# Optimization experiments

Measured on AMD Instinct MI355X. Metric: run time of the kernel, lower is better.

Reference implementation:

```python
import jax, jax.numpy as jnp
import numpy as np
import math

B, S, H, NH = 2, 2048, 2048, 16
HD = H // NH
BASE = 10000.0


def _rope_tables():
    inv_freq = 1.0 / (BASE ** (np.arange(0, HD, 2, dtype=np.float32) / HD))
    t = np.arange(S, dtype=np.float32)
    freqs = np.einsum('i,j->ij', t, inv_freq)          # [S, HD/2]
    emb = np.concatenate([freqs, freqs], axis=-1)       # [S, HD]
    return jnp.asarray(np.cos(emb)), jnp.asarray(np.sin(emb))


def setup_inputs() -> dict:
    key = jax.random.key(0)
    ks = jax.random.split(key, 6)
    scale = 1.0 / math.sqrt(H)
    cos, sin = _rope_tables()
    causal = np.triu(np.full((S, S), -1e9, dtype=np.float32), k=1)
    attn_bias = jnp.broadcast_to(jnp.asarray(causal)[None, None], (B, 1, S, S))
    return {
        'hidden_states': jax.random.normal(ks[0], (B, S, H), jnp.float32),
        'masks': jnp.zeros((B, S, S), jnp.float32),
        'attn_bias': attn_bias,
        'cos': cos,
        'sin': sin,
        'wq': jax.random.normal(ks[1], (H, H), jnp.float32) * scale,
        'wk': jax.random.normal(ks[2], (H, H), jnp.float32) * scale,
        'wv': jax.random.normal(ks[3], (H, H), jnp.float32) * scale,
        'wo': jax.random.normal(ks[4], (H, H), jnp.float32) * scale,
        'position_ids': jnp.broadcast_to(jnp.arange(S, dtype=jnp.int64)[None], (B, S)),
    }


def _rotate_half(x):
    x1, x2 = x[..., : x.shape[-1] // 2], x[..., x.shape[-1] // 2:]
    return jnp.concatenate([-x2, x1], axis=-1)


def reference(hidden_states, masks, attn_bias, cos, sin, wq, wk, wv, wo, position_ids):
    b, s, h = hidden_states.shape
    nh, hd = NH, HD
    # QKV projections (torch Linear: x @ W.T), split heads -> [b, nh, s, hd]
    def proj(w):
        return (hidden_states @ w.T).reshape(b, s, nh, hd).transpose(0, 2, 1, 3)
    q, k, v = proj(wq), proj(wk), proj(wv)
    # RoPE
    cos_p = cos[position_ids][:, None]  # [b, 1, s, hd]
    sin_p = sin[position_ids][:, None]
    q = q * cos_p + _rotate_half(q) * sin_p
    k = k * cos_p + _rotate_half(k) * sin_p
    # attention scores with additive masks (mx_attn branch, fp math)
    att = jnp.einsum('bhqd,bhkd->bhqk', q / math.sqrt(hd), k)
    att = att + attn_bias + masks[:, None]
    att = jax.nn.softmax(att, axis=-1)
    out = jnp.einsum('bhqk,bhkd->bhqd', att, v)
    out = out.transpose(0, 2, 1, 3).reshape(b, s, h)
    return out @ wo.T
```

## Files before the change

kernel.cpp:

```cpp
#include <hip/hip_runtime.h>
#include <stdint.h>

#define B_  2
#define S_  2048
#define H_  2048
#define NH_ 16
#define HD_ 128

typedef __bf16 v8bf __attribute__((ext_vector_type(8)));
typedef float  v4f  __attribute__((ext_vector_type(4)));

__device__ __forceinline__ float b2f(unsigned short u) {
  union { unsigned int i; float f; } x; x.i = ((unsigned int)u) << 16; return x.f;
}
__device__ __forceinline__ unsigned short f2b(float f) {
  union { float f; unsigned int i; } x; x.f = f;
  unsigned int r = x.i + 0x7FFFu + ((x.i >> 16) & 1u);
  return (unsigned short)(r >> 16);
}

__device__ __forceinline__ void async16(const void* g, void* l) {
  __builtin_amdgcn_global_load_lds(
      (const __attribute__((address_space(1))) void*)g,
      (__attribute__((address_space(3))) void*)l, 16, 0, 0);
}

__global__ __launch_bounds__(256) void cvt_f32_bf16(const float* __restrict__ src,
                                                    unsigned short* __restrict__ dst,
                                                    int n4) {
  int i = blockIdx.x * 256 + threadIdx.x;
  if (i < n4) {
    float4 f = *(const float4*)(src + (size_t)i * 4);
    ushort4 u;
    u.x = f2b(f.x); u.y = f2b(f.y); u.z = f2b(f.z); u.w = f2b(f.w);
    *(ushort4*)(dst + (size_t)i * 4) = u;
  }
}

__device__ __forceinline__ void gemm_tile_nt(const unsigned short* __restrict__ A,
                                             const unsigned short* __restrict__ Bm,
                                             int m0, int n0, int Kdim,
                                             unsigned short* As, unsigned short* Bs,
                                             v4f (&acc)[4][4]) {
  const int tid = threadIdx.x;
  const int lane = tid & 63, w = tid >> 6;
  const int lr = lane & 15, lg = lane >> 4;
  const int wm = (w >> 1) * 64, wn = (w & 1) * 64;

  for (int k0 = 0; k0 < Kdim; k0 += 32) {
    __syncthreads();
#pragma unroll
    for (int i = 0; i < 2; ++i) {
      const int cbase = i * 256 + w * 64;
      const int cc = cbase + lane;
      const int row = cc >> 2, col = (cc & 3) << 3;
      async16(A  + (size_t)(m0 + row) * Kdim + k0 + col, (char*)As + (size_t)cbase * 16);
      async16(Bm + (size_t)(n0 + row) * Kdim + k0 + col, (char*)Bs + (size_t)cbase * 16);
    }
    __syncthreads();
    v8bf a[4], bb[4];
#pragma unroll
    for (int i = 0; i < 4; i++) a[i]  = *(const v8bf*)(As + (wm + i * 16 + lr) * 32 + lg * 8);
#pragma unroll
    for (int i = 0; i < 4; i++) bb[i] = *(const v8bf*)(Bs + (wn + i * 16 + lr) * 32 + lg * 8);
#pragma unroll
    for (int mi = 0; mi < 4; mi++)
#pragma unroll
      for (int ni = 0; ni < 4; ni++)
        acc[mi][ni] = __builtin_amdgcn_mfma_f32_16x16x32_bf16(a[mi], bb[ni], acc[mi][ni], 0, 0, 0);
  }
}

__global__ __launch_bounds__(256, 2) void gemm_qkv(const unsigned short* __restrict__ X,
                                                   const unsigned short* __restrict__ Wq,
                                                   const unsigned short* __restrict__ Wk,
                                                   const unsigned short* __restrict__ Wv,
                                                   unsigned short* __restrict__ Qo,
                                                   unsigned short* __restrict__ Ko,
                                                   unsigned short* __restrict__ Vo) {
  __shared__ unsigned short As[128 * 32], Bs[128 * 32];
  const int m0 = blockIdx.x * 128;
  const int ny = blockIdx.y;
  const int sel = ny >> 4;
  const unsigned short* Bm = (sel == 0) ? Wq : (sel == 1 ? Wk : Wv);
  unsigned short* Out = (sel == 0) ? Qo : (sel == 1 ? Ko : Vo);
  const int n0 = (ny & 15) * 128;

  v4f acc[4][4];
#pragma unroll
  for (int i = 0; i < 4; i++)
#pragma unroll
    for (int j = 0; j < 4; j++) { v4f z = {0.f, 0.f, 0.f, 0.f}; acc[i][j] = z; }

  gemm_tile_nt(X, Bm, m0, n0, H_, As, Bs, acc);

  const int lane = threadIdx.x & 63, w = threadIdx.x >> 6;
  const int lr = lane & 15, lg = lane >> 4;
  const int wm = (w >> 1) * 64, wn = (w & 1) * 64;
#pragma unroll
  for (int mi = 0; mi < 4; mi++)
#pragma unroll
    for (int ni = 0; ni < 4; ni++)
#pragma unroll
      for (int r = 0; r < 4; r++)
        Out[(size_t)(m0 + wm + mi * 16 + lg * 4 + r) * H_ + n0 + wn + ni * 16 + lr] =
            f2b(acc[mi][ni][r]);
}

__global__ __launch_bounds__(256, 2) void gemm_out(const unsigned short* __restrict__ A,
                                                   const unsigned short* __restrict__ Wo,
                                                   float* __restrict__ Out) {
  __shared__ unsigned short As[128 * 32], Bs[128 * 32];
  const int m0 = blockIdx.x * 128;
  const int n0 = blockIdx.y * 128;

  v4f acc[4][4];
#pragma unroll
  for (int i = 0; i < 4; i++)
#pragma unroll
    for (int j = 0; j < 4; j++) { v4f z = {0.f, 0.f, 0.f, 0.f}; acc[i][j] = z; }

  gemm_tile_nt(A, Wo, m0, n0, H_, As, Bs, acc);

  const int lane = threadIdx.x & 63, w = threadIdx.x >> 6;
  const int lr = lane & 15, lg = lane >> 4;
  const int wm = (w >> 1) * 64, wn = (w & 1) * 64;
#pragma unroll
  for (int mi = 0; mi < 4; mi++)
#pragma unroll
    for (int ni = 0; ni < 4; ni++)
#pragma unroll
      for (int r = 0; r < 4; r++)
        Out[(size_t)(m0 + wm + mi * 16 + lg * 4 + r) * H_ + n0 + wn + ni * 16 + lr] =
            acc[mi][ni][r];
}

__global__ __launch_bounds__(256) void rope_kernel(unsigned short* __restrict__ Q,
                                                   unsigned short* __restrict__ K,
                                                   const float* __restrict__ cosT,
                                                   const float* __restrict__ sinT) {
  unsigned idx = blockIdx.x * 256 + threadIdx.x;
  int dq = (idx & 15) * 4;
  int h  = (idx >> 4) & 15;
  int s  = (idx >> 8) & 2047;
  int b  = idx >> 19;
  size_t base = ((size_t)(b * S_ + s)) * H_ + h * HD_;
  const float* cr = cosT + (size_t)s * HD_;
  const float* sr = sinT + (size_t)s * HD_;
  float c1[4], c2[4], s1[4], s2[4];
#pragma unroll
  for (int j = 0; j < 4; j++) {
    c1[j] = cr[dq + j]; c2[j] = cr[64 + dq + j];
    s1[j] = sr[dq + j]; s2[j] = sr[64 + dq + j];
  }
#pragma unroll
  for (int a = 0; a < 2; a++) {
    unsigned short* P = a == 0 ? Q : K;
    const float sc = (a == 0) ? (float)(0.08838834764831845 * 1.4426950408889634) : 1.0f;
    ushort4 u1 = *(ushort4*)(P + base + dq);
    ushort4 u2 = *(ushort4*)(P + base + 64 + dq);
    float x1[4] = {b2f(u1.x), b2f(u1.y), b2f(u1.z), b2f(u1.w)};
    float x2[4] = {b2f(u2.x), b2f(u2.y), b2f(u2.z), b2f(u2.w)};
    ushort4 o1, o2;
    o1.x = f2b((x1[0] * c1[0] - x2[0] * s1[0]) * sc);
    o1.y = f2b((x1[1] * c1[1] - x2[1] * s1[1]) * sc);
    o1.z = f2b((x1[2] * c1[2] - x2[2] * s1[2]) * sc);
    o1.w = f2b((x1[3] * c1[3] - x2[3] * s1[3]) * sc);
    o2.x = f2b((x2[0] * c2[0] + x1[0] * s2[0]) * sc);
    o2.y = f2b((x2[1] * c2[1] + x1[1] * s2[1]) * sc);
    o2.z = f2b((x2[2] * c2[2] + x1[2] * s2[2]) * sc);
    o2.w = f2b((x2[3] * c2[3] + x1[3] * s2[3]) * sc);
    *(ushort4*)(P + base + dq) = o1;
    *(ushort4*)(P + base + 64 + dq) = o2;
  }
}

__global__ __launch_bounds__(256) void transpose_v(const unsigned short* __restrict__ Vb,
                                                   unsigned short* __restrict__ Vt) {
  __shared__ unsigned short tile[64][130];
  const int tid = threadIdx.x;
  const int s0 = blockIdx.x * 64;
  const int h = blockIdx.y, b = blockIdx.z;
  for (int i = tid; i < 64 * 64; i += 256) {
    int s = i >> 6, dp = i & 63;
    *(ushort2*)&tile[s][dp * 2] =
        *(const ushort2*)(Vb + (size_t)(b * S_ + s0 + s) * H_ + h * HD_ + dp * 2);
  }
  __syncthreads();
  for (int i = tid; i < 128 * 64; i += 256) {
    int d = i >> 6, s = i & 63;
    Vt[((size_t)((b * NH_ + h) * HD_) + d) * S_ + s0 + s] = tile[s][d];
  }
}

#define KT_ 64

__global__ __launch_bounds__(512, 2) void attn_kernel(const unsigned short* __restrict__ Qb,
                                                      const unsigned short* __restrict__ Kb,
                                                      const unsigned short* __restrict__ Vt,
                                                      unsigned short* __restrict__ Ob) {
  __shared__ __align__(16) char smem[54272];
  unsigned short* Ks = (unsigned short*)smem;
  unsigned short* Vs = (unsigned short*)(smem + 17408);
  unsigned short* Ps = (unsigned short*)(smem + 35840);

  const int tid = threadIdx.x, lane = tid & 63, w = tid >> 6;
  const int lr = lane & 15, lg = lane >> 4;
  const int qp = blockIdx.x, h = blockIdx.y, b = blockIdx.z;

#pragma unroll 1
  for (int pass = 0; pass < 2; pass++) {
    const int qt = pass ? (15 - qp) : qp;
    const int q0 = qt * 128;
    const int wrow = q0 + w * 16;

    v8bf qf[4];
#pragma unroll
    for (int ks = 0; ks < 4; ks++)
      qf[ks] = *(const v8bf*)(Qb + (size_t)(b * S_ + wrow + lr) * H_ +
                              h * HD_ + ks * 32 + lg * 8);

    v4f o[8];
#pragma unroll
    for (int nt = 0; nt < 8; nt++) { v4f z = {0.f, 0.f, 0.f, 0.f}; o[nt] = z; }
    float mst[4], lst[4];
#pragma unroll
    for (int r = 0; r < 4; r++) { mst[r] = -1e30f; lst[r] = 0.f; }

    const int nkt = (q0 + 128) / KT_;
    for (int kt = 0; kt < nkt; kt++) {
      const int k0 = kt * KT_;
      __syncthreads();
#pragma unroll
      for (int i = 0; i < 3; ++i) {
        int cbase = i * 512 + w * 64;
        if (cbase < 1088) {
          int cc = cbase + lane;
          int row = cc / 17, pos = cc % 17;
          int p2 = (pos == 16) ? 0 : pos;
          async16(Kb + (size_t)(b * S_ + k0 + row) * H_ + h * HD_ + p2 * 8,
                  (char*)Ks + (size_t)cbase * 16);
        }
      }
#pragma unroll
      for (int i = 0; i < 3; ++i) {
        int cbase = i * 512 + w * 64;
        if (cbase < 1152) {
          int cc = cbase + lane;
          int row = cc / 9, pos = cc % 9;
          int p2 = (pos == 8) ? 0 : pos;
          async16(Vt + ((size_t)((b * NH_ + h) * HD_ + row)) * S_ + k0 + p2 * 8,
                  (char*)Vs + (size_t)cbase * 16);
        }
      }
      __syncthreads();

      if (k0 <= wrow + 15) {
        v4f sacc[4];
#pragma unroll
        for (int nt = 0; nt < 4; nt++) { v4f z = {0.f, 0.f, 0.f, 0.f}; sacc[nt] = z; }
#pragma unroll
        for (int nt = 0; nt < 4; nt++) {
          v8bf kf[4];
#pragma unroll
          for (int ks = 0; ks < 4; ks++)
            kf[ks] = *(const v8bf*)(Ks + (nt * 16 + lr) * 136 + ks * 32 + lg * 8);
#pragma unroll
          for (int ks = 0; ks < 4; ks++)
            sacc[nt] =
                __builtin_amdgcn_mfma_f32_16x16x32_bf16(qf[ks], kf[ks], sacc[nt], 0, 0, 0);
        }
        if (k0 + KT_ - 1 > wrow) {
#pragma unroll
          for (int nt = 0; nt < 4; nt++)
#pragma unroll
            for (int r = 0; r < 4; r++) {
              int key = k0 + nt * 16 + lr;
              int query = wrow + lg * 4 + r;
              if (key > query) sacc[nt][r] = -1e30f;
            }
        }
        float rmax[4], alpha[4], rsum[4];
#pragma unroll
        for (int r = 0; r < 4; r++) {
          float v = fmaxf(fmaxf(sacc[0][r], sacc[1][r]),
                          fmaxf(sacc[2][r], sacc[3][r]));
#pragma unroll
          for (int off = 8; off >= 1; off >>= 1) v = fmaxf(v, __shfl_xor(v, off, 64));
          rmax[r] = v;
        }
#pragma unroll
        for (int r = 0; r < 4; r++) {
          float mnew = fmaxf(mst[r], rmax[r]);
          alpha[r] = exp2f(mst[r] - mnew);
          mst[r] = mnew;
          rsum[r] = 0.f;
        }
#pragma unroll
        for (int nt = 0; nt < 4; nt++)
#pragma unroll
          for (int r = 0; r < 4; r++) {
            float p = exp2f(sacc[nt][r] - mst[r]);
            rsum[r] += p;
            Ps[w * 1152 + (lg * 4 + r) * 72 + nt * 16 + lr] = f2b(p);
          }
#pragma unroll
        for (int r = 0; r < 4; r++) {
#pragma unroll
          for (int off = 8; off >= 1; off >>= 1) rsum[r] += __shfl_xor(rsum[r], off, 64);
          lst[r] = lst[r] * alpha[r] + rsum[r];
        }
#pragma unroll
        for (int nt = 0; nt < 8; nt++)
#pragma unroll
          for (int r = 0; r < 4; r++) o[nt][r] *= alpha[r];
        asm volatile("" ::: "memory");
        v8bf af[2];
#pragma unroll
        for (int ks = 0; ks < 2; ks++)
          af[ks] = *(const v8bf*)(Ps + w * 1152 + lr * 72 + ks * 32 + lg * 8);
#pragma unroll
        for (int nt = 0; nt < 8; nt++) {
          v8bf bv[2];
#pragma unroll
          for (int ks = 0; ks < 2; ks++)
            bv[ks] = *(const v8bf*)(Vs + (nt * 16 + lr) * 72 + ks * 32 + lg * 8);
#pragma unroll
          for (int ks = 0; ks < 2; ks++)
            o[nt] = __builtin_amdgcn_mfma_f32_16x16x32_bf16(af[ks], bv[ks], o[nt], 0, 0, 0);
        }
      }
    }
    float inv[4];
#pragma unroll
    for (int r = 0; r < 4; r++) inv[r] = 1.f / lst[r];
#pragma unroll
    for (int nt = 0; nt < 8; nt++)
#pragma unroll
      for (int r = 0; r < 4; r++) {
        int row = wrow + lg * 4 + r;
        int col = h * HD_ + nt * 16 + lr;
        Ob[(size_t)(b * S_ + row) * H_ + col] = f2b(o[nt][r] * inv[r]);
      }
    __syncthreads();
  }
}

extern "C" void kernel_launch(void* const* d_in, const int* in_sizes, int n_in,
                              void* d_out, int out_size, void* d_ws, size_t ws_size,
                              hipStream_t stream) {
  const float* hidden = (const float*)d_in[0];
  const float* cosT = (const float*)d_in[3];
  const float* sinT = (const float*)d_in[4];
  const float* wq = (const float*)d_in[5];
  const float* wk = (const float*)d_in[6];
  const float* wv = (const float*)d_in[7];
  const float* wo = (const float*)d_in[8];
  float* out = (float*)d_out;

  char* p = (char*)d_ws;
  const size_t SZ_X = (size_t)4096 * 2048 * 2;
  const size_t SZ_W = (size_t)2048 * 2048 * 2;
  unsigned short* Xb  = (unsigned short*)p; p += SZ_X;
  unsigned short* Wqb = (unsigned short*)p; p += SZ_W;
  unsigned short* Wkb = (unsigned short*)p; p += SZ_W;
  unsigned short* Wvb = (unsigned short*)p; p += SZ_W;
  unsigned short* Wob = (unsigned short*)p; p += SZ_W;
  unsigned short* Qb  = (unsigned short*)p; p += SZ_X;
  unsigned short* Kb  = (unsigned short*)p; p += SZ_X;
  unsigned short* Vb  = (unsigned short*)p; p += SZ_X;
  unsigned short* Vt  = (unsigned short*)p; p += SZ_X;
  unsigned short* Ob  = Vb;

  cvt_f32_bf16<<<8192, 256, 0, stream>>>(hidden, Xb, 2097152);
  cvt_f32_bf16<<<4096, 256, 0, stream>>>(wq, Wqb, 1048576);
  cvt_f32_bf16<<<4096, 256, 0, stream>>>(wk, Wkb, 1048576);
  cvt_f32_bf16<<<4096, 256, 0, stream>>>(wv, Wvb, 1048576);
  cvt_f32_bf16<<<4096, 256, 0, stream>>>(wo, Wob, 1048576);

  gemm_qkv<<<dim3(32, 48), 256, 0, stream>>>(Xb, Wqb, Wkb, Wvb, Qb, Kb, Vb);
  rope_kernel<<<4096, 256, 0, stream>>>(Qb, Kb, cosT, sinT);
  transpose_v<<<dim3(32, 16, 2), 256, 0, stream>>>(Vb, Vt);
  attn_kernel<<<dim3(8, 16, 2), 512, 0, stream>>>(Qb, Kb, Vt, Ob);
  gemm_out<<<dim3(32, 16), 256, 0, stream>>>(Ob, Wob, out);
}
```

Baseline: 470.4 us.

## Fuse conversion and post-QKV kernels, pad GEMM LDS rows, truncate P to bf16

Merges the five fp32-to-bf16 conversion launches into one kernel and fuses RoPE with the V transpose into a single launch to cut launch overhead. Pads the GEMM shared-memory tiles to a 40-element row stride, filled with one extra duplicated chunk per row, to reduce LDS bank conflicts on fragment reads. Replaces round-to-nearest with truncation when converting softmax probabilities to bf16, which slightly changes numerics. The padding adds extra async loads per K step.

Result: no change. 465.9 us (-1.0%).

```diff
diff --git a/kernel.cpp b/kernel.cpp
--- a/kernel.cpp
+++ b/kernel.cpp
@@ -25,17 +25,35 @@
       (__attribute__((address_space(3))) void*)l, 16, 0, 0);
 }
 
-__global__ __launch_bounds__(256) void cvt_f32_bf16(const float* __restrict__ src,
-                                                    unsigned short* __restrict__ dst,
-                                                    int n4) {
-  int i = blockIdx.x * 256 + threadIdx.x;
-  if (i < n4) {
-    float4 f = *(const float4*)(src + (size_t)i * 4);
-    ushort4 u;
-    u.x = f2b(f.x); u.y = f2b(f.y); u.z = f2b(f.z); u.w = f2b(f.w);
-    *(ushort4*)(dst + (size_t)i * 4) = u;
-  }
-}
+__global__ __launch_bounds__(256) void cvt_all(const float* __restrict__ hid,
+                                               const float* __restrict__ wq,
+                                               const float* __restrict__ wk,
+                                               const float* __restrict__ wv,
+                                               const float* __restrict__ wo,
+                                               unsigned short* __restrict__ Xb,
+                                               unsigned short* __restrict__ Wqb,
+                                               unsigned short* __restrict__ Wkb,
+                                               unsigned short* __restrict__ Wvb,
+                                               unsigned short* __restrict__ Wob) {
+  int bid = blockIdx.x;
+  const float* src;
+  unsigned short* dst;
+  int rel;
+  if (bid < 8192)       { src = hid; dst = Xb;  rel = bid; }
+  else if (bid < 12288) { src = wq;  dst = Wqb; rel = bid - 8192; }
+  else if (bid < 16384) { src = wk;  dst = Wkb; rel = bid - 12288; }
+  else if (bid < 20480) { src = wv;  dst = Wvb; rel = bid - 16384; }
+  else                  { src = wo;  dst = Wob; rel = bid - 20480; }
+  int i = rel * 256 + threadIdx.x;
+  float4 f = *(const float4*)(src + (size_t)i * 4);
+  ushort4 u;
+  u.x = f2b(f.x); u.y = f2b(f.y); u.z = f2b(f.z); u.w = f2b(f.w);
+  *(ushort4*)(dst + (size_t)i * 4) = u;
+}
+
+#define ROWCH 5
+#define ROWU  (ROWCH * 8)
+#define NCHK  (128 * ROWCH)
 
 __device__ __forceinline__ void gemm_tile_nt(const unsigned short* __restrict__ A,
                                              const unsigned short* __restrict__ Bm,
@@ -50,19 +68,23 @@
   for (int k0 = 0; k0 < Kdim; k0 += 32) {
     __syncthreads();
 #pragma unroll
-    for (int i = 0; i < 2; ++i) {
+    for (int i = 0; i < 3; ++i) {
       const int cbase = i * 256 + w * 64;
-      const int cc = cbase + lane;
-      const int row = cc >> 2, col = (cc & 3) << 3;
-      async16(A  + (size_t)(m0 + row) * Kdim + k0 + col, (char*)As + (size_t)cbase * 16);
-      async16(Bm + (size_t)(n0 + row) * Kdim + k0 + col, (char*)Bs + (size_t)cbase * 16);
+      if (cbase < NCHK) {
+        const int cc = cbase + lane;
+        const int row = (cc * 205) >> 10;
+        const int pos = cc - row * 5;
+        const int p2 = (pos == 4) ? 0 : pos;
+        async16(A  + (size_t)(m0 + row) * Kdim + k0 + p2 * 8, (char*)As + (size_t)cbase * 16);
+        async16(Bm + (size_t)(n0 + row) * Kdim + k0 + p2 * 8, (char*)Bs + (size_t)cbase * 16);
+      }
     }
     __syncthreads();
     v8bf a[4], bb[4];
 #pragma unroll
-    for (int i = 0; i < 4; i++) a[i]  = *(const v8bf*)(As + (wm + i * 16 + lr) * 32 + lg * 8);
-#pragma unroll
-    for (int i = 0; i < 4; i++) bb[i] = *(const v8bf*)(Bs + (wn + i * 16 + lr) * 32 + lg * 8);
+    for (int i = 0; i < 4; i++) a[i]  = *(const v8bf*)(As + (wm + i * 16 + lr) * ROWU + lg * 8);
+#pragma unroll
+    for (int i = 0; i < 4; i++) bb[i] = *(const v8bf*)(Bs + (wn + i * 16 + lr) * ROWU + lg * 8);
 #pragma unroll
     for (int mi = 0; mi < 4; mi++)
 #pragma unroll
@@ -78,7 +100,7 @@
                                                    unsigned short* __restrict__ Qo,
                                                    unsigned short* __restrict__ Ko,
                                                    unsigned short* __restrict__ Vo) {
-  __shared__ unsigned short As[128 * 32], Bs[128 * 32];
+  __shared__ unsigned short As[NCHK * 8], Bs[NCHK * 8];
   const int m0 = blockIdx.x * 128;
   const int ny = blockIdx.y;
   const int sel = ny >> 4;
@@ -110,7 +132,7 @@
 __global__ __launch_bounds__(256, 2) void gemm_out(const unsigned short* __restrict__ A,
                                                    const unsigned short* __restrict__ Wo,
                                                    float* __restrict__ Out) {
-  __shared__ unsigned short As[128 * 32], Bs[128 * 32];
+  __shared__ unsigned short As[NCHK * 8], Bs[NCHK * 8];
   const int m0 = blockIdx.x * 128;
   const int n0 = blockIdx.y * 128;
 
@@ -135,61 +157,64 @@
             acc[mi][ni][r];
 }
 
-__global__ __launch_bounds__(256) void rope_kernel(unsigned short* __restrict__ Q,
-                                                   unsigned short* __restrict__ K,
-                                                   const float* __restrict__ cosT,
-                                                   const float* __restrict__ sinT) {
-  unsigned idx = blockIdx.x * 256 + threadIdx.x;
-  int dq = (idx & 15) * 4;
-  int h  = (idx >> 4) & 15;
-  int s  = (idx >> 8) & 2047;
-  int b  = idx >> 19;
-  size_t base = ((size_t)(b * S_ + s)) * H_ + h * HD_;
-  const float* cr = cosT + (size_t)s * HD_;
-  const float* sr = sinT + (size_t)s * HD_;
-  float c1[4], c2[4], s1[4], s2[4];
-#pragma unroll
-  for (int j = 0; j < 4; j++) {
-    c1[j] = cr[dq + j]; c2[j] = cr[64 + dq + j];
-    s1[j] = sr[dq + j]; s2[j] = sr[64 + dq + j];
-  }
-#pragma unroll
-  for (int a = 0; a < 2; a++) {
-    unsigned short* P = a == 0 ? Q : K;
-    const float sc = (a == 0) ? (float)(0.08838834764831845 * 1.4426950408889634) : 1.0f;
-    ushort4 u1 = *(ushort4*)(P + base + dq);
-    ushort4 u2 = *(ushort4*)(P + base + 64 + dq);
-    float x1[4] = {b2f(u1.x), b2f(u1.y), b2f(u1.z), b2f(u1.w)};
-    float x2[4] = {b2f(u2.x), b2f(u2.y), b2f(u2.z), b2f(u2.w)};
-    ushort4 o1, o2;
-    o1.x = f2b((x1[0] * c1[0] - x2[0] * s1[0]) * sc);
-    o1.y = f2b((x1[1] * c1[1] - x2[1] * s1[1]) * sc);
-    o1.z = f2b((x1[2] * c1[2] - x2[2] * s1[2]) * sc);
-    o1.w = f2b((x1[3] * c1[3] - x2[3] * s1[3]) * sc);
-    o2.x = f2b((x2[0] * c2[0] + x1[0] * s2[0]) * sc);
-    o2.y = f2b((x2[1] * c2[1] + x1[1] * s2[1]) * sc);
-    o2.z = f2b((x2[2] * c2[2] + x1[2] * s2[2]) * sc);
-    o2.w = f2b((x2[3] * c2[3] + x1[3] * s2[3]) * sc);
-    *(ushort4*)(P + base + dq) = o1;
-    *(ushort4*)(P + base + 64 + dq) = o2;
-  }
-}
-
-__global__ __launch_bounds__(256) void transpose_v(const unsigned short* __restrict__ Vb,
-                                                   unsigned short* __restrict__ Vt) {
+__global__ __launch_bounds__(256) void post_qkv(unsigned short* __restrict__ Q,
+                                                unsigned short* __restrict__ K,
+                                                const float* __restrict__ cosT,
+                                                const float* __restrict__ sinT,
+                                                const unsigned short* __restrict__ Vb,
+                                                unsigned short* __restrict__ Vt) {
   __shared__ unsigned short tile[64][130];
-  const int tid = threadIdx.x;
-  const int s0 = blockIdx.x * 64;
-  const int h = blockIdx.y, b = blockIdx.z;
-  for (int i = tid; i < 64 * 64; i += 256) {
-    int s = i >> 6, dp = i & 63;
-    *(ushort2*)&tile[s][dp * 2] =
-        *(const ushort2*)(Vb + (size_t)(b * S_ + s0 + s) * H_ + h * HD_ + dp * 2);
-  }
-  __syncthreads();
-  for (int i = tid; i < 128 * 64; i += 256) {
-    int d = i >> 6, s = i & 63;
-    Vt[((size_t)((b * NH_ + h) * HD_) + d) * S_ + s0 + s] = tile[s][d];
+  const int bid = blockIdx.x;
+  if (bid < 4096) {
+    unsigned idx = bid * 256 + threadIdx.x;
+    int dq = (idx & 15) * 4;
+    int h  = (idx >> 4) & 15;
+    int s  = (idx >> 8) & 2047;
+    int b  = idx >> 19;
+    size_t base = ((size_t)(b * S_ + s)) * H_ + h * HD_;
+    const float* cr = cosT + (size_t)s * HD_;
+    const float* sr = sinT + (size_t)s * HD_;
+    float c1[4], c2[4], s1[4], s2[4];
+#pragma unroll
+    for (int j = 0; j < 4; j++) {
+      c1[j] = cr[dq + j]; c2[j] = cr[64 + dq + j];
+      s1[j] = sr[dq + j]; s2[j] = sr[64 + dq + j];
+    }
+#pragma unroll
+    for (int a = 0; a < 2; a++) {
+      unsigned short* P = a == 0 ? Q : K;
+      const float sc = (a == 0) ? (float)(0.08838834764831845 * 1.4426950408889634) : 1.0f;
+      ushort4 u1 = *(ushort4*)(P + base + dq);
+      ushort4 u2 = *(ushort4*)(P + base + 64 + dq);
+      float x1[4] = {b2f(u1.x), b2f(u1.y), b2f(u1.z), b2f(u1.w)};
+      float x2[4] = {b2f(u2.x), b2f(u2.y), b2f(u2.z), b2f(u2.w)};
+      ushort4 o1, o2;
+      o1.x = f2b((x1[0] * c1[0] - x2[0] * s1[0]) * sc);
+      o1.y = f2b((x1[1] * c1[1] - x2[1] * s1[1]) * sc);
+      o1.z = f2b((x1[2] * c1[2] - x2[2] * s1[2]) * sc);
+      o1.w = f2b((x1[3] * c1[3] - x2[3] * s1[3]) * sc);
+      o2.x = f2b((x2[0] * c2[0] + x1[0] * s2[0]) * sc);
+      o2.y = f2b((x2[1] * c2[1] + x1[1] * s2[1]) * sc);
+      o2.z = f2b((x2[2] * c2[2] + x1[2] * s2[2]) * sc);
+      o2.w = f2b((x2[3] * c2[3] + x1[3] * s2[3]) * sc);
+      *(ushort4*)(P + base + dq) = o1;
+      *(ushort4*)(P + base + 64 + dq) = o2;
+    }
+  } else {
+    const int tb = bid - 4096;
+    const int tid = threadIdx.x;
+    const int s0 = (tb & 31) * 64;
+    const int h = (tb >> 5) & 15, b = tb >> 9;
+    for (int i = tid; i < 64 * 64; i += 256) {
+      int s = i >> 6, dp = i & 63;
+      *(ushort2*)&tile[s][dp * 2] =
+          *(const ushort2*)(Vb + (size_t)(b * S_ + s0 + s) * H_ + h * HD_ + dp * 2);
+    }
+    __syncthreads();
+    for (int i = tid; i < 128 * 64; i += 256) {
+      int d = i >> 6, s = i & 63;
+      Vt[((size_t)((b * NH_ + h) * HD_) + d) * S_ + s0 + s] = tile[s][d];
+    }
   }
 }
 
@@ -302,7 +327,9 @@
           for (int r = 0; r < 4; r++) {
             float p = exp2f(sacc[nt][r] - mst[r]);
             rsum[r] += p;
-            Ps[w * 1152 + (lg * 4 + r) * 72 + nt * 16 + lr] = f2b(p);
+            union { float f; unsigned u; } pu; pu.f = p;
+            Ps[w * 1152 + (lg * 4 + r) * 72 + nt * 16 + lr] =
+                (unsigned short)(pu.u >> 16);
           }
 #pragma unroll
         for (int r = 0; r < 4; r++) {
@@ -372,15 +399,9 @@
   unsigned short* Vt  = (unsigned short*)p; p += SZ_X;
   unsigned short* Ob  = Vb;
 
-  cvt_f32_bf16<<<8192, 256, 0, stream>>>(hidden, Xb, 2097152);
-  cvt_f32_bf16<<<4096, 256, 0, stream>>>(wq, Wqb, 1048576);
-  cvt_f32_bf16<<<4096, 256, 0, stream>>>(wk, Wkb, 1048576);
-  cvt_f32_bf16<<<4096, 256, 0, stream>>>(wv, Wvb, 1048576);
-  cvt_f32_bf16<<<4096, 256, 0, stream>>>(wo, Wob, 1048576);
-
+  cvt_all<<<24576, 256, 0, stream>>>(hidden, wq, wk, wv, wo, Xb, Wqb, Wkb, Wvb, Wob);
   gemm_qkv<<<dim3(32, 48), 256, 0, stream>>>(Xb, Wqb, Wkb, Wvb, Qb, Kb, Vb);
-  rope_kernel<<<4096, 256, 0, stream>>>(Qb, Kb, cosT, sinT);
-  transpose_v<<<dim3(32, 16, 2), 256, 0, stream>>>(Vb, Vt);
+  post_qkv<<<5120, 256, 0, stream>>>(Qb, Kb, cosT, sinT, Vb, Vt);
   attn_kernel<<<dim3(8, 16, 2), 512, 0, stream>>>(Qb, Kb, Vt, Ob);
   gemm_out<<<dim3(32, 16), 256, 0, stream>>>(Ob, Wob, out);
 }
```
